# Kernel optimization log

Hardware: AMD Instinct MI355X
Metric: run time of the kernel (lower is better)

The kernel has to match this reference:

```python
import jax, jax.numpy as jnp
import numpy as np
import math

LN_EPS = 1e-5
EPS = 1e-8

def _unfold3(x, stride):
    # torch nn.Unfold(kernel_size=3, stride=stride, padding=1); output [B, C*9, L]
    B, C, H, W = x.shape
    xp = jnp.pad(x, ((0, 0), (0, 0), (1, 1), (1, 1)))
    Ho = (H + 2 - 3) // stride + 1
    Wo = (W + 2 - 3) // stride + 1
    pats = [xp[:, :, i:i + stride * (Ho - 1) + 1:stride, j:j + stride * (Wo - 1) + 1:stride]
            for i in range(3) for j in range(3)]
    out = jnp.stack(pats, axis=2)  # [B,C,9,Ho,Wo]  (c-major, then kh,kw: torch ordering)
    return out.reshape(B, C * 9, Ho * Wo)

def _ln(x, g, b):
    mu = jnp.mean(x, axis=-1, keepdims=True)
    var = jnp.mean((x - mu) ** 2, axis=-1, keepdims=True)
    return (x - mu) * jax.lax.rsqrt(var + LN_EPS) * g + b

def _prm_exp(x, w):
    # x: [B,T,emb], w: [m,emb] -> [B,T,m]
    m = w.shape[0]
    xd = jnp.sum(x * x, axis=-1, keepdims=True) / 2.0
    wtx = jnp.einsum('bte,me->btm', x, w)
    return jnp.exp(wtx - xd) / math.sqrt(m)

def _performer(x, kqv_w, kqv_b, pw, pb, g1, b1, g2, b2, m1w, m1b, m2w, m2b, w):
    # Token_performer.forward (dropout = identity, eval mode)
    h = _ln(x, g1, b1)
    kqv = h @ kqv_w.T + kqv_b
    k, q, v = jnp.split(kqv, 3, axis=-1)  # torch.split order: k, q, v
    kp = _prm_exp(k, w)
    qp = _prm_exp(q, w)
    D = jnp.einsum('btm,bm->bt', qp, kp.sum(axis=1))[..., None]        # [B,T,1]
    kptv = jnp.einsum('btn,btm->bnm', v, kp)                            # [B,emb,m]
    y = jnp.einsum('btm,bnm->btn', qp, kptv) / (D + EPS)                # [B,T,emb]
    y = v + (y @ pw.T + pb)
    h2 = _ln(y, g2, b2)
    mlp = jax.nn.gelu(h2 @ m1w.T + m1b, approximate=False) @ m2w.T + m2b
    return y + mlp

def _forward(x,
             p1_kqv_w, p1_kqv_b, p1_proj_w, p1_proj_b, p1_n1_g, p1_n1_b, p1_n2_g, p1_n2_b,
             p1_m1_w, p1_m1_b, p1_m2_w, p1_m2_b, p1_w,
             p2_kqv_w, p2_kqv_b, p2_proj_w, p2_proj_b, p2_n1_g, p2_n1_b, p2_n2_g, p2_n2_b,
             p2_m1_w, p2_m1_b, p2_m2_w, p2_m2_b, p2_w,
             proj_w, proj_b):
    t = _unfold3(x, 1).transpose(0, 2, 1)  # [B, 50176, 27]
    t = _performer(t, p1_kqv_w, p1_kqv_b, p1_proj_w, p1_proj_b, p1_n1_g, p1_n1_b,
                   p1_n2_g, p1_n2_b, p1_m1_w, p1_m1_b, p1_m2_w, p1_m2_b, p1_w)
    B, N, C = t.shape
    s = int(math.isqrt(N))
    t = t.transpose(0, 2, 1).reshape(B, C, s, s)
    t = _unfold3(t, 2).transpose(0, 2, 1)  # [B, 12544, 576]
    t = _performer(t, p2_kqv_w, p2_kqv_b, p2_proj_w, p2_proj_b, p2_n1_g, p2_n1_b,
                   p2_n2_g, p2_n2_b, p2_m1_w, p2_m1_b, p2_m2_w, p2_m2_b, p2_w)
    B, N, C = t.shape
    s = int(math.isqrt(N))
    t = t.transpose(0, 2, 1).reshape(B, C, s, s)
    t = _unfold3(t, 2).transpose(0, 2, 1)  # [B, 3136, 576]
    return t @ proj_w.T + proj_b           # [B, 3136, 768]

def setup_inputs() -> dict:
    key = jax.random.key(0)
    ks = iter(jax.random.split(key, 40))
    def rn(shape, scale=0.02):
        return (jax.random.normal(next(ks), shape, dtype=jnp.float32) * scale)
    EMB, M = 64, 32
    inp = {'x': jax.random.normal(next(ks), (8, 3, 224, 224), dtype=jnp.float32)}
    for pfx, dim in (('p1', 27), ('p2', 576)):
        inp[f'{pfx}_kqv_w'] = rn((3 * EMB, dim))
        inp[f'{pfx}_kqv_b'] = jnp.zeros((3 * EMB,), jnp.float32)
        inp[f'{pfx}_proj_w'] = rn((EMB, EMB))
        inp[f'{pfx}_proj_b'] = jnp.zeros((EMB,), jnp.float32)
        inp[f'{pfx}_n1_g'] = jnp.ones((dim,), jnp.float32)
        inp[f'{pfx}_n1_b'] = jnp.zeros((dim,), jnp.float32)
        inp[f'{pfx}_n2_g'] = jnp.ones((EMB,), jnp.float32)
        inp[f'{pfx}_n2_b'] = jnp.zeros((EMB,), jnp.float32)
        inp[f'{pfx}_m1_w'] = rn((EMB, EMB))
        inp[f'{pfx}_m1_b'] = jnp.zeros((EMB,), jnp.float32)
        inp[f'{pfx}_m2_w'] = rn((EMB, EMB))
        inp[f'{pfx}_m2_b'] = jnp.zeros((EMB,), jnp.float32)
        # frozen random-feature projection, scaled ~ orthogonal * sqrt(m)
        inp[f'{pfx}_w'] = jax.random.normal(next(ks), (M, EMB), dtype=jnp.float32)
    inp['proj_w'] = rn((768, 576))
    inp['proj_b'] = jnp.zeros((768,), jnp.float32)
    return inp

def reference(x,
              p1_kqv_w, p1_kqv_b, p1_proj_w, p1_proj_b, p1_n1_g, p1_n1_b, p1_n2_g, p1_n2_b,
              p1_m1_w, p1_m1_b, p1_m2_w, p1_m2_b, p1_w,
              p2_kqv_w, p2_kqv_b, p2_proj_w, p2_proj_b, p2_n1_g, p2_n1_b, p2_n2_g, p2_n2_b,
              p2_m1_w, p2_m1_b, p2_m2_w, p2_m2_b, p2_w,
              proj_w, proj_b):
    return _forward(x,
                    p1_kqv_w, p1_kqv_b, p1_proj_w, p1_proj_b, p1_n1_g, p1_n1_b, p1_n2_g, p1_n2_b,
                    p1_m1_w, p1_m1_b, p1_m2_w, p1_m2_b, p1_w,
                    p2_kqv_w, p2_kqv_b, p2_proj_w, p2_proj_b, p2_n1_g, p2_n1_b, p2_n2_g, p2_n2_b,
                    p2_m1_w, p2_m1_b, p2_m2_w, p2_m2_b, p2_w,
                    proj_w, proj_b)
```

## Files before the change

kernel.cpp:

```cpp
#include <hip/hip_runtime.h>
#include <hip/hip_bf16.h>
#include <math.h>

typedef __hip_bfloat16 bf16;
typedef __attribute__((ext_vector_type(8))) short frag8;
typedef __attribute__((ext_vector_type(4))) float f32x4;
typedef long long ll;

__device__ __forceinline__ float b2f(bf16 v) { return __bfloat162float(v); }
__device__ __forceinline__ bf16 f2b(float v) { return __float2bfloat16(v); }

__device__ __forceinline__ unsigned pk2f(float a, float b) {
    union { bf16 h[2]; unsigned u; } c;
    c.h[0] = f2b(a); c.h[1] = f2b(b);
    return c.u;
}
__device__ __forceinline__ void up8(const bf16* p, float* f) {
    const uint4 u = *(const uint4*)p;
    union { unsigned u; bf16 h[2]; } c;
    c.u = u.x; f[0] = b2f(c.h[0]); f[1] = b2f(c.h[1]);
    c.u = u.y; f[2] = b2f(c.h[0]); f[3] = b2f(c.h[1]);
    c.u = u.z; f[4] = b2f(c.h[0]); f[5] = b2f(c.h[1]);
    c.u = u.w; f[6] = b2f(c.h[0]); f[7] = b2f(c.h[1]);
}

#define LN_EPS 1e-5f
#define D_EPS 1e-8f
#define INV_SQRT_M 0.17677669529663687f

__global__ __launch_bounds__(256) void k_sniff(const void* x, int* mode)
{
    __shared__ int cnt;
    if (threadIdx.x == 0) cnt = 0;
    __syncthreads();
    const unsigned short* u = (const unsigned short*)x;
    const unsigned short h = u[2 * threadIdx.x];
    const unsigned int bits = ((unsigned int)h) << 16;
    const float v = __uint_as_float(bits);
    const float a = fabsf(v);
    const bool sane = (h == 0) || (a >= 1e-8f && a <= 1e4f);
    if (!sane) atomicAdd(&cnt, 1);
    __syncthreads();
    if (threadIdx.x == 0) *mode = (cnt > 64) ? 1 : 0;
}

struct CvTab { const void* src[28]; int dstOff[28]; int cum[29]; };

__global__ __launch_bounds__(256) void k_convert_all(CvTab tab, bf16* base,
                                                     const int* mode)
{
    const int idx = blockIdx.x * 256 + threadIdx.x;
    if (idx >= tab.cum[28]) return;
    int s = 0;
    while (idx >= tab.cum[s + 1]) ++s;
    const int local = idx - tab.cum[s];
    const float v = (*mode) ? ((const float*)tab.src[s])[local]
                            : b2f(((const bf16*)tab.src[s])[local]);
    base[tab.dstOff[s] + local] = f2b(v);
}

__global__ __launch_bounds__(256) void k_prep(
    const void* __restrict__ w1raw, const int* __restrict__ mode,
    bf16* __restrict__ w1ph, bf16* __restrict__ w1pl)
{
    const int idx = blockIdx.x * 256 + threadIdx.x;
    if (idx >= 6144) return;
    const int o = idx >> 5, k = idx & 31;
    float v = 0.f;
    if (k < 27)
        v = (*mode) ? ((const float*)w1raw)[o * 27 + k]
                    : b2f(((const bf16*)w1raw)[o * 27 + k]);
    const bf16 h = f2b(v);
    w1ph[idx] = h;
    w1pl[idx] = f2b(v - b2f(h));
}

__global__ __launch_bounds__(256) void k_fused1(
    const bf16* __restrict__ x, const bf16* __restrict__ w1ph,
    const bf16* __restrict__ w1pl, const bf16* __restrict__ kqvb,
    const bf16* __restrict__ n1g, const bf16* __restrict__ n1b,
    const bf16* __restrict__ pw,
    bf16* __restrict__ KP, bf16* __restrict__ QP, bf16* __restrict__ V,
    float* __restrict__ red, const int b)
{
    __shared__ __align__(16) char smem[49632];
    bf16 (*wps)[72] = (bf16(*)[72])(smem);
    bf16 (*Ah)[40]  = (bf16(*)[40])(smem + 4608);
    bf16 (*Al)[40]  = (bf16(*)[40])(smem + 9728);
    bf16 (*Th)[72]  = (bf16(*)[72])(smem + 14848);
    bf16 (*Tl)[72]  = (bf16(*)[72])(smem + 24064);
    bf16 (*Wh)[40]  = (bf16(*)[40])(smem + 33280);
    bf16 (*Wl)[40]  = (bf16(*)[40])(smem + 38400);
    bf16 (*KPs)[40] = (bf16(*)[40])(smem + 43520);
    bf16 (*Vs)[72]  = (bf16(*)[72])(smem + 14848);
    float* kbs = (float*)(smem + 48640);
    float* gs  = (float*)(smem + 49408);
    float* bs  = (float*)(smem + 49520);

    const int tid = threadIdx.x;
    {
        const int i = tid * 8;
        *(uint4*)(&wps[i >> 6][i & 63]) = *(const uint4*)(pw + i);
    }
    if (tid < 192) kbs[tid] = b2f(kqvb[tid]);
    if (tid < 27) { gs[tid] = b2f(n1g[tid]); bs[tid] = b2f(n1b[tid]); }
    if (blockIdx.x == 0)
        for (int i = tid; i < 2080; i += 256) red[i] = 0.f;

    const int tok = tid >> 2, part = tid & 3;
    const int t = blockIdx.x * 64 + tok;
    const int h = t / 224, w = t - h * 224;
    const int d0 = part * 7;
    const int nd = (part == 3) ? 6 : 7;
    float vals[7];
    float s = 0.f;
    #pragma unroll
    for (int q = 0; q < 7; ++q) {
        float val = 0.f;
        if (q < nd) {
            const int d = d0 + q;
            const int c = d / 9, rr = d - c * 9;
            const int pi = rr / 3, pj = rr - pi * 3;
            const int hh = h + pi - 1, ww = w + pj - 1;
            if (hh >= 0 && hh < 224 && ww >= 0 && ww < 224)
                val = b2f(x[((ll)(b * 3 + c) * 224 + hh) * 224 + ww]);
        }
        vals[q] = val; s += val;
    }
    s += __shfl_xor(s, 1, 64);  s += __shfl_xor(s, 2, 64);
    const float mean = s * (1.f / 27.f);
    float s2 = 0.f;
    #pragma unroll
    for (int q = 0; q < 7; ++q) {
        if (q < nd) { const float dd = vals[q] - mean; s2 += dd * dd; }
    }
    s2 += __shfl_xor(s2, 1, 64); s2 += __shfl_xor(s2, 2, 64);
    const float rs = rsqrtf(s2 * (1.f / 27.f) + LN_EPS);
    __syncthreads();
    #pragma unroll
    for (int q = 0; q < 7; ++q) {
        if (q < nd) {
            const int d = d0 + q;
            const float nv = (vals[q] - mean) * rs * gs[d] + bs[d];
            const bf16 nh = f2b(nv);
            Ah[tok][d] = nh;
            Al[tok][d] = f2b(nv - b2f(nh));
        }
    }
    if (part == 3) {
        #pragma unroll
        for (int d = 27; d < 32; ++d) { Ah[tok][d] = f2b(0.f); Al[tok][d] = f2b(0.f); }
    }

    const int wv = tid >> 6, lane = tid & 63;
    const int l15 = lane & 15;
    const int k8 = (lane >> 4) << 3;
    const int rbase = (lane >> 4) << 2;
    const int srow = tid >> 2;
    const int scol = (tid & 3) << 3;
    const int colg = (tid & 3) << 4;

    float xdK[4], xdQ[4];

    #pragma unroll
    for (int g = 0; g < 3; ++g) {
        *(uint4*)(&Wh[srow][scol]) = *(const uint4*)(w1ph + (g * 64 + srow) * 32 + scol);
        *(uint4*)(&Wl[srow][scol]) = *(const uint4*)(w1pl + (g * 64 + srow) * 32 + scol);
        __syncthreads();
        const frag8 ah = *(const frag8*)(&Ah[(wv << 4) + l15][k8]);
        const frag8 al = *(const frag8*)(&Al[(wv << 4) + l15][k8]);
        f32x4 acc[4] = {};
        #pragma unroll
        for (int nt = 0; nt < 4; ++nt) {
            const frag8 bh = *(const frag8*)(&Wh[(nt << 4) + l15][k8]);
            const frag8 bl = *(const frag8*)(&Wl[(nt << 4) + l15][k8]);
            acc[nt] = __builtin_amdgcn_mfma_f32_16x16x32_bf16(ah, bh, acc[nt], 0, 0, 0);
            acc[nt] = __builtin_amdgcn_mfma_f32_16x16x32_bf16(al, bh, acc[nt], 0, 0, 0);
            acc[nt] = __builtin_amdgcn_mfma_f32_16x16x32_bf16(ah, bl, acc[nt], 0, 0, 0);
            acc[nt] = __builtin_amdgcn_mfma_f32_16x16x32_bf16(al, bl, acc[nt], 0, 0, 0);
        }
        float xdp[4] = {0.f, 0.f, 0.f, 0.f};
        #pragma unroll
        for (int nt = 0; nt < 4; ++nt) {
            const int col = (nt << 4) + l15;
            const float bv = kbs[g * 64 + col];
            #pragma unroll
            for (int r = 0; r < 4; ++r) {
                const float tb = acc[nt][r] + bv;
                const int trow = (wv << 4) + rbase + r;
                if (g < 2) {
                    const bf16 th = f2b(tb);
                    Th[trow][col] = th;
                    Tl[trow][col] = f2b(tb - b2f(th));
                    xdp[r] += tb * tb;
                } else {
                    Vs[trow][col] = f2b(tb);
                }
            }
        }
        if (g < 2) {
            #pragma unroll
            for (int r = 0; r < 4; ++r) {
                float v = xdp[r];
                v += __shfl_xor(v, 1, 64); v += __shfl_xor(v, 2, 64);
                v += __shfl_xor(v, 4, 64); v += __shfl_xor(v, 8, 64);
                if (g == 0) xdK[r] = 0.5f * v; else xdQ[r] = 0.5f * v;
            }
        }
        __syncthreads();
        if (g < 2) {
            f32x4 acc2[2] = {};
            #pragma unroll
            for (int k0 = 0; k0 < 64; k0 += 32) {
                const frag8 ath = *(const frag8*)(&Th[(wv << 4) + l15][k8 + k0]);
                const frag8 atl = *(const frag8*)(&Tl[(wv << 4) + l15][k8 + k0]);
                #pragma unroll
                for (int nt = 0; nt < 2; ++nt) {
                    const frag8 bw = *(const frag8*)(&wps[(nt << 4) + l15][k8 + k0]);
                    acc2[nt] = __builtin_amdgcn_mfma_f32_16x16x32_bf16(ath, bw, acc2[nt], 0, 0, 0);
                    acc2[nt] = __builtin_amdgcn_mfma_f32_16x16x32_bf16(atl, bw, acc2[nt], 0, 0, 0);
                }
            }
            #pragma unroll
            for (int nt = 0; nt < 2; ++nt)
                #pragma unroll
                for (int r = 0; r < 4; ++r) {
                    const float xd = (g == 0) ? xdK[r] : xdQ[r];
                    const float p = expf(fminf(acc2[nt][r] - xd, 30.f)) * INV_SQRT_M;
                    KPs[(wv << 4) + rbase + r][(nt << 4) + l15] = f2b(p);
                }
            __syncthreads();
            bf16* dstP = (g == 0 ? KP : QP) + ((ll)blockIdx.x * 64 + srow) * 32 + scol;
            *(uint4*)dstP = *(const uint4*)(&KPs[srow][scol]);
            __syncthreads();
        } else {
            bf16* dstV = V + ((ll)blockIdx.x * 64 + srow) * 64 + colg;
            *(uint4*)dstV       = *(const uint4*)(&Vs[srow][colg]);
            *(uint4*)(dstV + 8) = *(const uint4*)(&Vs[srow][colg + 8]);
        }
    }
}

__global__ __launch_bounds__(256) void k_reduce(
    const bf16* __restrict__ kpB, const bf16* __restrict__ vB, const int vstride,
    const int T, float* __restrict__ redBase, const int chunk)
{
    __shared__ bf16 VT[64][72];
    __shared__ bf16 KT[32][72];
    const int bz = blockIdx.y;
    const bf16* kp = kpB + (ll)bz * T * 32;
    const bf16* v  = vB + (ll)bz * T * (ll)vstride;
    float* red = redBase + (ll)bz * 2080;
    const int tid = threadIdx.x;
    const int wv = tid >> 6, lane = tid & 63;
    const int l15 = lane & 15, k8 = (lane >> 4) << 3, rbase = (lane >> 4) << 2;
    const int t0 = blockIdx.x * chunk;

    frag8 ones;
    {
        union { bf16 h; short s; } u; u.h = f2b(1.f);
        #pragma unroll
        for (int i = 0; i < 8; ++i) ones[i] = u.s;
    }

    f32x4 acc[2] = {};
    f32x4 accK[2] = {};

    for (int tt = 0; tt < chunk; tt += 64) {
        const int tb = t0 + tt;
        __syncthreads();
        {
            const int tk = tid >> 2, n0 = (tid & 3) << 4;
            const bf16* src = v + (ll)(tb + tk) * vstride + n0;
            bf16 tmp[16];
            *(uint4*)tmp       = *(const uint4*)src;
            *(uint4*)(tmp + 8) = *(const uint4*)(src + 8);
            #pragma unroll
            for (int j = 0; j < 16; ++j) VT[n0 + j][tk] = tmp[j];
        }
        {
            const int tk = tid >> 2, m0 = (tid & 3) << 3;
            const bf16* src = kp + (ll)(tb + tk) * 32 + m0;
            bf16 tmp[8];
            *(uint4*)tmp = *(const uint4*)src;
            #pragma unroll
            for (int j = 0; j < 8; ++j) KT[m0 + j][tk] = tmp[j];
        }
        __syncthreads();
        #pragma unroll
        for (int ks = 0; ks < 2; ++ks) {
            const frag8 af = *(const frag8*)(&VT[(wv << 4) + l15][k8 + ks * 32]);
            #pragma unroll
            for (int tn = 0; tn < 2; ++tn) {
                const frag8 bfv = *(const frag8*)(&KT[(tn << 4) + l15][k8 + ks * 32]);
                acc[tn] = __builtin_amdgcn_mfma_f32_16x16x32_bf16(af, bfv, acc[tn], 0, 0, 0);
            }
            if (wv == 0) {
                #pragma unroll
                for (int tn = 0; tn < 2; ++tn) {
                    const frag8 bfv = *(const frag8*)(&KT[(tn << 4) + l15][k8 + ks * 32]);
                    accK[tn] = __builtin_amdgcn_mfma_f32_16x16x32_bf16(ones, bfv, accK[tn], 0, 0, 0);
                }
            }
        }
    }
    #pragma unroll
    for (int tn = 0; tn < 2; ++tn) {
        const int m = (tn << 4) + l15;
        #pragma unroll
        for (int r = 0; r < 4; ++r) {
            const int n = (wv << 4) + rbase + r;
            atomicAdd(&red[n * 32 + m], acc[tn][r]);
        }
    }
    if (wv == 0 && (lane >> 4) == 0) {
        #pragma unroll
        for (int tn = 0; tn < 2; ++tn)
            atomicAdd(&red[2048 + (tn << 4) + l15], accK[tn][0]);
    }
}

__global__ __launch_bounds__(256) void k_posta(
    const bf16* __restrict__ qpB, const float* __restrict__ redBase,
    const bf16* __restrict__ vB, const int vstride,
    const bf16* __restrict__ pw, const bf16* __restrict__ pb,
    bf16* outB, const int T)
{
    __shared__ __align__(16) char smem[46720];
    bf16 (*QPs)[40] = (bf16(*)[40])(smem);
    bf16 (*KH)[40]  = (bf16(*)[40])(smem + 5120);
    bf16 (*KL)[40]  = (bf16(*)[40])(smem + 10240);
    float (*Cs)[72] = (float(*)[72])(smem);
    bf16 (*PWs)[72] = (bf16(*)[72])(smem + 18432);
    bf16 (*Y0H)[72] = (bf16(*)[72])(smem + 27648);
    bf16 (*Y0L)[72] = (bf16(*)[72])(smem + 36864);
    float* invs  = (float*)(smem + 46080);
    float* pbs   = (float*)(smem + 46336);
    float* ksums = (float*)(smem + 46592);

    const int tid = threadIdx.x;
    const int bz = blockIdx.y;
    const float* red = redBase + (ll)bz * 2080;
    const bf16* qp = qpB + (ll)bz * (ll)T * 32;
    const bf16* v  = vB + (ll)bz * (ll)T * (ll)vstride;
    bf16* out = outB + (ll)bz * (ll)T * 64;
    const ll m0 = (ll)blockIdx.x * 64;

    {
        const int lr = tid >> 2, lc = (tid & 3) << 3;
        *(uint4*)(&QPs[lr][lc]) = *(const uint4*)(qp + (m0 + lr) * 32 + lc);
    }
    {
        const int lr = tid >> 2, lc = (tid & 3) << 4;
        *(uint4*)(&PWs[lr][lc])     = *(const uint4*)(pw + lr * 64 + lc);
        *(uint4*)(&PWs[lr][lc + 8]) = *(const uint4*)(pw + lr * 64 + lc + 8);
    }
    {
        const int i0 = tid * 8;
        const float4 a = *(const float4*)(red + i0);
        const float4 b = *(const float4*)(red + i0 + 4);
        const int n = i0 >> 5, m = i0 & 31;
        float xs[8] = {a.x, a.y, a.z, a.w, b.x, b.y, b.z, b.w};
        #pragma unroll
        for (int k = 0; k < 8; ++k) {
            const bf16 h = f2b(xs[k]);
            KH[n][m + k] = h;
            KL[n][m + k] = f2b(xs[k] - b2f(h));
        }
    }
    if (tid < 32) ksums[tid] = red[2048 + tid];
    if (tid < 64) pbs[tid] = b2f(pb[tid]);
    __syncthreads();

    if (tid < 64) {
        float D = D_EPS;
        #pragma unroll
        for (int m = 0; m < 32; ++m) D += b2f(QPs[tid][m]) * ksums[m];
        invs[tid] = 1.f / D;
    }

    const int wv = tid >> 6, lane = tid & 63;
    const int mr = (wv << 4) + (lane & 15);
    const int k8 = (lane >> 4) << 3;
    const int rbase = (lane >> 4) << 2;

    f32x4 acc[4] = {};
    {
        const frag8 af = *(const frag8*)(&QPs[mr][k8]);
        #pragma unroll
        for (int tn = 0; tn < 4; ++tn) {
            const int nr = (tn << 4) + (lane & 15);
            const frag8 bh = *(const frag8*)(&KH[nr][k8]);
            acc[tn] = __builtin_amdgcn_mfma_f32_16x16x32_bf16(af, bh, acc[tn], 0, 0, 0);
            const frag8 bl = *(const frag8*)(&KL[nr][k8]);
            acc[tn] = __builtin_amdgcn_mfma_f32_16x16x32_bf16(af, bl, acc[tn], 0, 0, 0);
        }
    }
    #pragma unroll
    for (int tn = 0; tn < 4; ++tn) {
        const int n = (tn << 4) + (lane & 15);
        #pragma unroll
        for (int r = 0; r < 4; ++r) {
            const float x = acc[tn][r];
            const bf16 h = f2b(x);
            Y0H[(wv << 4) + rbase + r][n] = h;
            Y0L[(wv << 4) + rbase + r][n] = f2b(x - b2f(h));
        }
    }
    __syncthreads();

    f32x4 acc2[4] = {};
    #pragma unroll
    for (int k0 = 0; k0 < 64; k0 += 32) {
        const frag8 ah = *(const frag8*)(&Y0H[mr][k8 + k0]);
        const frag8 al = *(const frag8*)(&Y0L[mr][k8 + k0]);
        #pragma unroll
        for (int tn = 0; tn < 4; ++tn) {
            const frag8 bw = *(const frag8*)(&PWs[(tn << 4) + (lane & 15)][k8 + k0]);
            acc2[tn] = __builtin_amdgcn_mfma_f32_16x16x32_bf16(ah, bw, acc2[tn], 0, 0, 0);
            acc2[tn] = __builtin_amdgcn_mfma_f32_16x16x32_bf16(al, bw, acc2[tn], 0, 0, 0);
        }
    }
    #pragma unroll
    for (int tn = 0; tn < 4; ++tn) {
        const int n = (tn << 4) + (lane & 15);
        #pragma unroll
        for (int r = 0; r < 4; ++r) {
            const int row = (wv << 4) + rbase + r;
            Cs[row][n] = acc2[tn][r] * invs[row] + pbs[n];
        }
    }
    __syncthreads();

    const int row = tid >> 2;
    const int colg = (tid & 3) << 4;
    const bf16* vsrc = v + (m0 + row) * (ll)vstride + colg;
    bf16* dst = out + (m0 + row) * 64 + colg;
    #pragma unroll
    for (int hh = 0; hh < 2; ++hh) {
        float vv[8];
        up8(vsrc + hh * 8, vv);
        const float* cp = &Cs[row][colg + hh * 8];
        uint4 st;
        st.x = pk2f(cp[0] + vv[0], cp[1] + vv[1]);
        st.y = pk2f(cp[2] + vv[2], cp[3] + vv[3]);
        st.z = pk2f(cp[4] + vv[4], cp[5] + vv[5]);
        st.w = pk2f(cp[6] + vv[6], cp[7] + vv[7]);
        *(uint4*)(dst + hh * 8) = st;
    }
}

__global__ __launch_bounds__(256) void k_mlpln(
    const bf16* H, const bf16* __restrict__ n2g, const bf16* __restrict__ n2b,
    const bf16* __restrict__ w1, const bf16* __restrict__ b1,
    const bf16* __restrict__ w2, const bf16* __restrict__ b2,
    const bf16* res, bf16* out)
{
    __shared__ bf16 Hs[64][72];
    __shared__ bf16 W1s[64][72];
    __shared__ bf16 W2s[64][72];
    __shared__ bf16 Gs[64][72];
    __shared__ float mns[64], rss[64];
    const int tid = threadIdx.x;
    const int wv = tid >> 6, lane = tid & 63;
    const ll m0 = (ll)blockIdx.x * 64;
    const int lr = tid >> 2;
    const int lc = (tid & 3) << 4;
    *(uint4*)(&Hs[lr][lc])      = *(const uint4*)(H + (m0 + lr) * 64 + lc);
    *(uint4*)(&Hs[lr][lc + 8])  = *(const uint4*)(H + (m0 + lr) * 64 + lc + 8);
    *(uint4*)(&W1s[lr][lc])     = *(const uint4*)(w1 + lr * 64 + lc);
    *(uint4*)(&W1s[lr][lc + 8]) = *(const uint4*)(w1 + lr * 64 + lc + 8);
    *(uint4*)(&W2s[lr][lc])     = *(const uint4*)(w2 + lr * 64 + lc);
    *(uint4*)(&W2s[lr][lc + 8]) = *(const uint4*)(w2 + lr * 64 + lc + 8);
    __syncthreads();
    if (tid < 64) {
        float s = 0.f, s2 = 0.f;
        #pragma unroll
        for (int n = 0; n < 64; ++n) { const float vv = b2f(Hs[tid][n]); s += vv; s2 += vv * vv; }
        const float mn = s * (1.f / 64.f);
        const float var = fmaxf(s2 * (1.f / 64.f) - mn * mn, 0.f);
        mns[tid] = mn; rss[tid] = rsqrtf(var + LN_EPS);
    }
    __syncthreads();
    for (int i = tid; i < 4096; i += 256) {
        const int r = i >> 6, c = i & 63;
        Hs[r][c] = f2b((b2f(Hs[r][c]) - mns[r]) * rss[r] * b2f(n2g[c]) + b2f(n2b[c]));
    }
    __syncthreads();
    const int mr = (wv << 4) + (lane & 15);
    const int k8 = (lane >> 4) << 3;
    const int rbase = (lane >> 4) << 2;
    f32x4 acc[4] = {};
    #pragma unroll
    for (int k0 = 0; k0 < 64; k0 += 32) {
        const frag8 af = *(const frag8*)(&Hs[mr][k8 + k0]);
        #pragma unroll
        for (int tn = 0; tn < 4; ++tn) {
            const frag8 bfv = *(const frag8*)(&W1s[(tn << 4) + (lane & 15)][k8 + k0]);
            acc[tn] = __builtin_amdgcn_mfma_f32_16x16x32_bf16(af, bfv, acc[tn], 0, 0, 0);
        }
    }
    #pragma unroll
    for (int tn = 0; tn < 4; ++tn) {
        const int n = (tn << 4) + (lane & 15);
        const float bv = b2f(b1[n]);
        #pragma unroll
        for (int r = 0; r < 4; ++r) {
            float v = acc[tn][r] + bv;
            v = 0.5f * v * (1.f + erff(v * 0.70710678118654752f));
            Gs[(wv << 4) + rbase + r][n] = f2b(v);
        }
    }
    __syncthreads();
    f32x4 acc2[4] = {};
    #pragma unroll
    for (int k0 = 0; k0 < 64; k0 += 32) {
        const frag8 af = *(const frag8*)(&Gs[mr][k8 + k0]);
        #pragma unroll
        for (int tn = 0; tn < 4; ++tn) {
            const frag8 bfv = *(const frag8*)(&W2s[(tn << 4) + (lane & 15)][k8 + k0]);
            acc2[tn] = __builtin_amdgcn_mfma_f32_16x16x32_bf16(af, bfv, acc2[tn], 0, 0, 0);
        }
    }
    #pragma unroll
    for (int tn = 0; tn < 4; ++tn) {
        const int n = (tn << 4) + (lane & 15);
        const float bv = b2f(b2[n]);
        #pragma unroll
        for (int r = 0; r < 4; ++r)
            Hs[(wv << 4) + rbase + r][n] = f2b(acc2[tn][r] + bv);
    }
    __syncthreads();
    const int row = tid >> 2;
    const int colg = (tid & 3) << 4;
    const bf16* rsrc = res + (m0 + row) * 64 + colg;
    bf16* dst = out + (m0 + row) * 64 + colg;
    #pragma unroll
    for (int hh = 0; hh < 2; ++hh) {
        float sv[8], rv[8];
        up8(&Hs[row][colg + hh * 8], sv);
        up8(rsrc + hh * 8, rv);
        uint4 st;
        st.x = pk2f(sv[0] + rv[0], sv[1] + rv[1]);
        st.y = pk2f(sv[2] + rv[2], sv[3] + rv[3]);
        st.z = pk2f(sv[4] + rv[4], sv[5] + rv[5]);
        st.w = pk2f(sv[6] + rv[6], sv[7] + rv[7]);
        *(uint4*)(dst + hh * 8) = st;
    }
}

__global__ __launch_bounds__(256) void k_unfold576(
    const bf16* __restrict__ in, const int Hin, const int Ho,
    const bf16* __restrict__ g, const bf16* __restrict__ bb,
    const int do_ln, bf16* __restrict__ A,
    const ll inBStride, const ll outBStride)
{
    in += (ll)blockIdx.y * inBStride;
    A  += (ll)blockIdx.y * outBStride;
    const int t = blockIdx.x * 4 + (threadIdx.x >> 6);
    const int l = threadIdx.x & 63;
    const int ho = t / Ho, wo = t - ho * Ho;
    float vals[9];
    float s = 0.f;
    #pragma unroll
    for (int r = 0; r < 9; ++r) {
        const int d = l + (r << 6);
        const int c = d / 9;
        const int rr = d - c * 9;
        const int i = rr / 3, j = rr - i * 3;
        const int hh = 2 * ho + i - 1, ww = 2 * wo + j - 1;
        float val = 0.f;
        if (hh >= 0 && hh < Hin && ww >= 0 && ww < Hin)
            val = b2f(in[((ll)hh * Hin + ww) * 64 + c]);
        vals[r] = val; s += val;
    }
    bf16* out = A + (ll)t * 576;
    if (do_ln) {
        #pragma unroll
        for (int o = 32; o > 0; o >>= 1) s += __shfl_xor(s, o, 64);
        const float mean = s * (1.f / 576.f);
        float s2 = 0.f;
        #pragma unroll
        for (int r = 0; r < 9; ++r) { const float dd = vals[r] - mean; s2 += dd * dd; }
        #pragma unroll
        for (int o = 32; o > 0; o >>= 1) s2 += __shfl_xor(s2, o, 64);
        const float rs = rsqrtf(s2 * (1.f / 576.f) + LN_EPS);
        #pragma unroll
        for (int r = 0; r < 9; ++r) {
            const int d = l + (r << 6);
            out[d] = f2b((vals[r] - mean) * rs * b2f(g[d]) + b2f(bb[d]));
        }
    } else {
        #pragma unroll
        for (int r = 0; r < 9; ++r) out[l + (r << 6)] = f2b(vals[r]);
    }
}

__global__ __launch_bounds__(256) void k_gemm(
    const bf16* __restrict__ A, const int lda,
    const bf16* __restrict__ W,
    const bf16* __restrict__ bias,
    const bf16* res, const int ldres,
    void* C, const int ldc, const ll mOff,
    const int K, const int* outm)
{
    __shared__ bf16 As[2][64][40];
    __shared__ bf16 Bs[2][64][40];
    __shared__ bf16 Cs[64][72];
    const int tid = threadIdx.x;
    const int wv = tid >> 6;
    const int lane = tid & 63;
    const ll m0 = (ll)blockIdx.x * 64;
    const int n0 = blockIdx.y * 64;
    f32x4 acc[4] = {};
    const int lr = tid >> 2;
    const int lc = (tid & 3) << 3;
    const int mr = (wv << 4) + (lane & 15);
    const int k8 = (lane >> 4) << 3;
    const bf16* Ag = A + (m0 + lr) * (ll)lda + lc;
    const bf16* Wg = W + (ll)(n0 + lr) * K + lc;

    uint4 av  = *(const uint4*)(Ag);
    uint4 wv4 = *(const uint4*)(Wg);
    *(uint4*)(&As[0][lr][lc]) = av;
    *(uint4*)(&Bs[0][lr][lc]) = wv4;
    int cur = 0;
    __syncthreads();
    for (int k0 = 0; k0 < K; k0 += 32) {
        const bool nxt = (k0 + 32 < K);
        if (nxt) {
            av  = *(const uint4*)(Ag + k0 + 32);
            wv4 = *(const uint4*)(Wg + k0 + 32);
        }
        const frag8 af = *(const frag8*)(&As[cur][mr][k8]);
        #pragma unroll
        for (int tn = 0; tn < 4; ++tn) {
            const frag8 bfv = *(const frag8*)(&Bs[cur][(tn << 4) + (lane & 15)][k8]);
            acc[tn] = __builtin_amdgcn_mfma_f32_16x16x32_bf16(af, bfv, acc[tn], 0, 0, 0);
        }
        if (nxt) {
            *(uint4*)(&As[cur ^ 1][lr][lc]) = av;
            *(uint4*)(&Bs[cur ^ 1][lr][lc]) = wv4;
        }
        __syncthreads();
        cur ^= 1;
    }
    const int om = outm ? *outm : 0;
    const int rbase = (lane >> 4) << 2;
    if (om) {
        #pragma unroll
        for (int tn = 0; tn < 4; ++tn) {
            const int n = n0 + (tn << 4) + (lane & 15);
            const float bv = bias ? b2f(bias[n]) : 0.f;
            #pragma unroll
            for (int r = 0; r < 4; ++r) {
                const ll m = m0 + (wv << 4) + rbase + r;
                float v = acc[tn][r] + bv;
                if (res) v += b2f(res[m * (ll)ldres + n]);
                ((float*)C)[(m + mOff) * (ll)ldc + n] = v;
            }
        }
        return;
    }
    #pragma unroll
    for (int tn = 0; tn < 4; ++tn) {
        const int nl = (tn << 4) + (lane & 15);
        const float bv = bias ? b2f(bias[n0 + nl]) : 0.f;
        #pragma unroll
        for (int r = 0; r < 4; ++r) {
            const ll m = m0 + (wv << 4) + rbase + r;
            float v = acc[tn][r] + bv;
            if (res) v += b2f(res[m * (ll)ldres + n0 + nl]);
            Cs[(wv << 4) + rbase + r][nl] = f2b(v);
        }
    }
    __syncthreads();
    const int row = tid >> 2;
    const int colg = (tid & 3) << 4;
    bf16* dst = (bf16*)C + (m0 + mOff + row) * (ll)ldc + n0 + colg;
    *(uint4*)dst       = *(const uint4*)(&Cs[row][colg]);
    *(uint4*)(dst + 8) = *(const uint4*)(&Cs[row][colg + 8]);
}

__global__ __launch_bounds__(256) void k_fusedP2(
    const bf16* __restrict__ kqv, const bf16* __restrict__ pw,
    bf16* __restrict__ KP, bf16* __restrict__ QP,
    float* __restrict__ redBase, const int T)
{
    __shared__ float wps[2048];
    const int tid = threadIdx.x;
    const int bz = blockIdx.y;
    for (int i = tid; i < 2048; i += 256) wps[i] = b2f(pw[i]);
    if (blockIdx.x == 0) {
        float* red = redBase + (ll)bz * 2080;
        for (int i = tid; i < 2080; i += 256) red[i] = 0.f;
    }
    __syncthreads();
    const ll gt = (ll)bz * T + blockIdx.x * 256 + tid;
    const bf16* row = kqv + gt * 192;
    float xv[64];
    float p32[32];
    #pragma unroll
    for (int g = 0; g < 8; ++g) up8(row + g * 8, xv + g * 8);
    float xd = 0.f;
    #pragma unroll
    for (int e = 0; e < 64; ++e) xd += xv[e] * xv[e];
    xd *= 0.5f;
    #pragma unroll 4
    for (int m = 0; m < 32; ++m) {
        float a = -xd;
        #pragma unroll
        for (int e = 0; e < 64; ++e) a += xv[e] * wps[m * 64 + e];
        p32[m] = expf(fminf(a, 30.f)) * INV_SQRT_M;
    }
    #pragma unroll
    for (int g = 0; g < 4; ++g) {
        uint4 st;
        st.x = pk2f(p32[g * 8 + 0], p32[g * 8 + 1]);
        st.y = pk2f(p32[g * 8 + 2], p32[g * 8 + 3]);
        st.z = pk2f(p32[g * 8 + 4], p32[g * 8 + 5]);
        st.w = pk2f(p32[g * 8 + 6], p32[g * 8 + 7]);
        *(uint4*)(KP + gt * 32 + g * 8) = st;
    }
    #pragma unroll
    for (int g = 0; g < 8; ++g) up8(row + 64 + g * 8, xv + g * 8);
    xd = 0.f;
    #pragma unroll
    for (int e = 0; e < 64; ++e) xd += xv[e] * xv[e];
    xd *= 0.5f;
    #pragma unroll 4
    for (int m = 0; m < 32; ++m) {
        float a = -xd;
        #pragma unroll
        for (int e = 0; e < 64; ++e) a += xv[e] * wps[m * 64 + e];
        p32[m] = expf(fminf(a, 30.f)) * INV_SQRT_M;
    }
    #pragma unroll
    for (int g = 0; g < 4; ++g) {
        uint4 st;
        st.x = pk2f(p32[g * 8 + 0], p32[g * 8 + 1]);
        st.y = pk2f(p32[g * 8 + 2], p32[g * 8 + 3]);
        st.z = pk2f(p32[g * 8 + 4], p32[g * 8 + 5]);
        st.w = pk2f(p32[g * 8 + 6], p32[g * 8 + 7]);
        *(uint4*)(QP + gt * 32 + g * 8) = st;
    }
}

extern "C" void kernel_launch(void* const* d_in, const int* in_sizes, int n_in,
                              void* d_out, int out_size, void* d_ws, size_t ws_size,
                              hipStream_t stream)
{
    (void)in_sizes; (void)n_in; (void)out_size; (void)ws_size;
    const int T1 = 50176, T2 = 12544;
    char* ws = (char*)d_ws;

    size_t cur = 0;
    auto alloc = [&](size_t bytes) {
        size_t r = cur; cur += (bytes + 127) & ~(size_t)127; return r;
    };
    static const int segIdx[28] = {0, 2, 3, 4, 5, 6, 7, 8, 9, 10, 11, 12, 13,
                                   14, 15, 16, 17, 18, 19, 20, 21, 22, 23, 24, 25, 26, 27, 28};
    static const int segN[28] = {1204224, 192, 4096, 64, 27, 27, 64, 64, 4096, 64, 4096, 64, 2048,
                                 110592, 192, 4096, 64, 576, 576, 64, 64, 4096, 64, 4096, 64, 2048,
                                 442368, 768};
    size_t segOff[28];
    for (int i = 0; i < 28; ++i) segOff[i] = alloc((size_t)segN[i] * 2);
    const size_t oMODE = alloc(256);
    const size_t oRED  = alloc(66560);
    const size_t oW1P  = alloc(24576);
    const size_t oBIG  = alloc(6422528);
    const size_t oKP   = alloc(3211264);
    const size_t oQP   = alloc(3211264);
    (void)oQP;

    bf16* P[28];
    for (int i = 0; i < 28; ++i) P[i] = (bf16*)(ws + segOff[i]);
    bf16* XC = P[0];
    bf16 *P1KQVB = P[1], *P1PW = P[2], *P1PB = P[3], *P1N1G = P[4], *P1N1B = P[5];
    bf16 *P1N2G = P[6], *P1N2B = P[7], *P1M1W = P[8], *P1M1B = P[9], *P1M2W = P[10];
    bf16 *P1M2B = P[11], *P1W = P[12];
    bf16 *P2KQVW = P[13], *P2KQVB = P[14], *P2PW = P[15], *P2PB = P[16];
    bf16 *P2N1G = P[17], *P2N1B = P[18], *P2N2G = P[19], *P2N2B = P[20];
    bf16 *P2M1W = P[21], *P2M1B = P[22], *P2M2W = P[23], *P2M2B = P[24], *P2W = P[25];
    bf16 *PROJW = P[26], *PROJB = P[27];

    int*   MODE = (int*)(ws + oMODE);
    float* REDF = (float*)(ws + oRED);
    bf16*  W1PH = (bf16*)(ws + oW1P);
    bf16*  W1PL = (bf16*)(ws + oW1P + 12288);
    bf16*  BIG  = (bf16*)(ws + oBIG);
    bf16*  KP   = (bf16*)(ws + oKP);
    bf16*  QP   = (bf16*)(ws + oKP + 3211264);
    bf16*  A2   = (bf16*)(ws + oKP);
    bf16*  KQV2F = (bf16*)d_out;
    bf16*  KP2F  = (bf16*)(ws + oKP);
    bf16*  QP2F  = (bf16*)(ws + oKP + 6422528);
    bf16*  YB2F  = (bf16*)(ws + oBIG);
    bf16*  A3c   = (bf16*)(ws + oBIG + 12845056);

    k_sniff<<<1, 256, 0, stream>>>(d_in[0], MODE);
    CvTab tab;
    int cum = 0;
    for (int i = 0; i < 28; ++i) {
        tab.src[i] = d_in[segIdx[i]];
        tab.dstOff[i] = (int)(segOff[i] / 2);
        tab.cum[i] = cum;
        cum += segN[i];
    }
    tab.cum[28] = cum;
    k_convert_all<<<(cum + 255) / 256, 256, 0, stream>>>(tab, (bf16*)ws, MODE);
    k_prep<<<24, 256, 0, stream>>>(d_in[1], MODE, W1PH, W1PL);

    for (int b = 0; b < 8; ++b) {
        float* REDb = REDF + (ll)b * 2080;
        k_fused1<<<784, 256, 0, stream>>>(XC, W1PH, W1PL, P1KQVB, P1N1G, P1N1B,
                                          P1W, KP, QP, BIG, REDb, b);
        k_reduce<<<dim3(392, 1), 256, 0, stream>>>(KP, BIG, 64, T1, REDb, 128);
        k_posta<<<dim3(784, 1), 256, 0, stream>>>(QP, REDb, BIG, 64, P1PW, P1PB,
                                                  BIG, T1);
        k_mlpln<<<784, 256, 0, stream>>>(BIG, P1N2G, P1N2B, P1M1W, P1M1B,
                                         P1M2W, P1M2B, BIG, BIG);
        k_unfold576<<<dim3(3136, 1), 256, 0, stream>>>(BIG, 224, 112, P2N1G, P2N1B,
                                                       1, A2, 0, 0);
        k_gemm<<<dim3(196, 3), 256, 0, stream>>>(A2, 576, P2KQVW, P2KQVB,
            nullptr, 0, KQV2F, 192, (ll)b * T2, 576, nullptr);
    }

    k_fusedP2<<<dim3(49, 8), 256, 0, stream>>>(KQV2F, P2W, KP2F, QP2F, REDF, T2);
    k_reduce<<<dim3(98, 8), 256, 0, stream>>>(KP2F, KQV2F + 128, 192, T2, REDF, 128);
    k_posta<<<dim3(196, 8), 256, 0, stream>>>(QP2F, REDF, KQV2F + 128, 192,
                                              P2PW, P2PB, YB2F, T2);
    k_mlpln<<<1568, 256, 0, stream>>>(YB2F, P2N2G, P2N2B, P2M1W, P2M1B,
                                      P2M2W, P2M2B, YB2F, YB2F);

    for (int c = 0; c < 4; ++c) {
        k_unfold576<<<dim3(784, 2), 256, 0, stream>>>(
            YB2F + (ll)(2 * c) * T2 * 64, 112, 56, nullptr, nullptr, 0,
            A3c, (ll)T2 * 64, (ll)3136 * 576);
        k_gemm<<<dim3(98, 12), 256, 0, stream>>>(A3c, 576, PROJW, PROJB,
            nullptr, 0, d_out, 768, (ll)c * 6272, 576, MODE);
    }
}
```

Baseline: 1.045 ms.

## Fuse attention post-process with MLP+LN, MFMA-ize stage-2 features, batch final projection

Merges k_posta and k_mlpln into one kernel that keeps the residual output in shared memory, removing a global round trip and a launch per stage. k_fusedP2 replaces its per-thread scalar 64x32 dot products with bf16 MFMA over 64-row tiles, run on a 4x larger grid. When the workspace is big enough, the final unfold+projection runs as one full-size launch instead of four chunks. The cost is more shared-memory aliasing, and the feature projection weights are now rounded to bf16 inside MFMA instead of being used in fp32.

```diff
diff --git a/kernel.cpp b/kernel.cpp
--- a/kernel.cpp
+++ b/kernel.cpp
@@ -17,6 +17,13 @@
 }
 __device__ __forceinline__ void up8(const bf16* p, float* f) {
     const uint4 u = *(const uint4*)p;
+    union { unsigned u; bf16 h[2]; } c;
+    c.u = u.x; f[0] = b2f(c.h[0]); f[1] = b2f(c.h[1]);
+    c.u = u.y; f[2] = b2f(c.h[0]); f[3] = b2f(c.h[1]);
+    c.u = u.z; f[4] = b2f(c.h[0]); f[5] = b2f(c.h[1]);
+    c.u = u.w; f[6] = b2f(c.h[0]); f[7] = b2f(c.h[1]);
+}
+__device__ __forceinline__ void up8u(const uint4 u, float* f) {
     union { unsigned u; bf16 h[2]; } c;
     c.u = u.x; f[0] = b2f(c.h[0]); f[1] = b2f(c.h[1]);
     c.u = u.y; f[2] = b2f(c.h[0]); f[3] = b2f(c.h[1]);
@@ -320,23 +327,33 @@
     }
 }
 
-__global__ __launch_bounds__(256) void k_posta(
+__global__ __launch_bounds__(256) void k_postmlp(
     const bf16* __restrict__ qpB, const float* __restrict__ redBase,
     const bf16* __restrict__ vB, const int vstride,
     const bf16* __restrict__ pw, const bf16* __restrict__ pb,
+    const bf16* __restrict__ n2g, const bf16* __restrict__ n2b,
+    const bf16* __restrict__ w1, const bf16* __restrict__ b1,
+    const bf16* __restrict__ w2, const bf16* __restrict__ b2,
     bf16* outB, const int T)
 {
-    __shared__ __align__(16) char smem[46720];
+    __shared__ __align__(16) char smem[47232];
     bf16 (*QPs)[40] = (bf16(*)[40])(smem);
     bf16 (*KH)[40]  = (bf16(*)[40])(smem + 5120);
     bf16 (*KL)[40]  = (bf16(*)[40])(smem + 10240);
     float (*Cs)[72] = (float(*)[72])(smem);
+    bf16 (*W1s)[72] = (bf16(*)[72])(smem);
+    bf16 (*W2s)[72] = (bf16(*)[72])(smem + 9216);
     bf16 (*PWs)[72] = (bf16(*)[72])(smem + 18432);
+    bf16 (*Gs)[72]  = (bf16(*)[72])(smem + 18432);
     bf16 (*Y0H)[72] = (bf16(*)[72])(smem + 27648);
+    bf16 (*Ys)[72]  = (bf16(*)[72])(smem + 27648);
     bf16 (*Y0L)[72] = (bf16(*)[72])(smem + 36864);
+    bf16 (*Hn)[72]  = (bf16(*)[72])(smem + 36864);
     float* invs  = (float*)(smem + 46080);
     float* pbs   = (float*)(smem + 46336);
     float* ksums = (float*)(smem + 46592);
+    float* mns   = (float*)(smem + 46720);
+    float* rss   = (float*)(smem + 46976);
 
     const int tid = threadIdx.x;
     const int bz = blockIdx.y;
@@ -346,15 +363,13 @@
     bf16* out = outB + (ll)bz * (ll)T * 64;
     const ll m0 = (ll)blockIdx.x * 64;
 
-    {
-        const int lr = tid >> 2, lc = (tid & 3) << 3;
-        *(uint4*)(&QPs[lr][lc]) = *(const uint4*)(qp + (m0 + lr) * 32 + lc);
-    }
-    {
-        const int lr = tid >> 2, lc = (tid & 3) << 4;
-        *(uint4*)(&PWs[lr][lc])     = *(const uint4*)(pw + lr * 64 + lc);
-        *(uint4*)(&PWs[lr][lc + 8]) = *(const uint4*)(pw + lr * 64 + lc + 8);
-    }
+    const int lr = tid >> 2;
+    const int lc8 = (tid & 3) << 3;
+    const int lc16 = (tid & 3) << 4;
+
+    *(uint4*)(&QPs[lr][lc8]) = *(const uint4*)(qp + (m0 + lr) * 32 + lc8);
+    *(uint4*)(&PWs[lr][lc16])     = *(const uint4*)(pw + lr * 64 + lc16);
+    *(uint4*)(&PWs[lr][lc16 + 8]) = *(const uint4*)(pw + lr * 64 + lc16 + 8);
     {
         const int i0 = tid * 8;
         const float4 a = *(const float4*)(red + i0);
@@ -380,7 +395,8 @@
     }
 
     const int wv = tid >> 6, lane = tid & 63;
-    const int mr = (wv << 4) + (lane & 15);
+    const int l15 = lane & 15;
+    const int mr = (wv << 4) + l15;
     const int k8 = (lane >> 4) << 3;
     const int rbase = (lane >> 4) << 2;
 
@@ -389,7 +405,7 @@
         const frag8 af = *(const frag8*)(&QPs[mr][k8]);
         #pragma unroll
         for (int tn = 0; tn < 4; ++tn) {
-            const int nr = (tn << 4) + (lane & 15);
+            const int nr = (tn << 4) + l15;
             const frag8 bh = *(const frag8*)(&KH[nr][k8]);
             acc[tn] = __builtin_amdgcn_mfma_f32_16x16x32_bf16(af, bh, acc[tn], 0, 0, 0);
             const frag8 bl = *(const frag8*)(&KL[nr][k8]);
@@ -398,7 +414,7 @@
     }
     #pragma unroll
     for (int tn = 0; tn < 4; ++tn) {
-        const int n = (tn << 4) + (lane & 15);
+        const int n = (tn << 4) + l15;
         #pragma unroll
         for (int r = 0; r < 4; ++r) {
             const float x = acc[tn][r];
@@ -416,14 +432,14 @@
         const frag8 al = *(const frag8*)(&Y0L[mr][k8 + k0]);
         #pragma unroll
         for (int tn = 0; tn < 4; ++tn) {
-            const frag8 bw = *(const frag8*)(&PWs[(tn << 4) + (lane & 15)][k8 + k0]);
+            const frag8 bw = *(const frag8*)(&PWs[(tn << 4) + l15][k8 + k0]);
             acc2[tn] = __builtin_amdgcn_mfma_f32_16x16x32_bf16(ah, bw, acc2[tn], 0, 0, 0);
             acc2[tn] = __builtin_amdgcn_mfma_f32_16x16x32_bf16(al, bw, acc2[tn], 0, 0, 0);
         }
     }
     #pragma unroll
     for (int tn = 0; tn < 4; ++tn) {
-        const int n = (tn << 4) + (lane & 15);
+        const int n = (tn << 4) + l15;
         #pragma unroll
         for (int r = 0; r < 4; ++r) {
             const int row = (wv << 4) + rbase + r;
@@ -432,120 +448,102 @@
     }
     __syncthreads();
 
-    const int row = tid >> 2;
-    const int colg = (tid & 3) << 4;
-    const bf16* vsrc = v + (m0 + row) * (ll)vstride + colg;
-    bf16* dst = out + (m0 + row) * 64 + colg;
-    #pragma unroll
-    for (int hh = 0; hh < 2; ++hh) {
-        float vv[8];
-        up8(vsrc + hh * 8, vv);
-        const float* cp = &Cs[row][colg + hh * 8];
-        uint4 st;
-        st.x = pk2f(cp[0] + vv[0], cp[1] + vv[1]);
-        st.y = pk2f(cp[2] + vv[2], cp[3] + vv[3]);
-        st.z = pk2f(cp[4] + vv[4], cp[5] + vv[5]);
-        st.w = pk2f(cp[6] + vv[6], cp[7] + vv[7]);
-        *(uint4*)(dst + hh * 8) = st;
-    }
-}
-
-__global__ __launch_bounds__(256) void k_mlpln(
-    const bf16* H, const bf16* __restrict__ n2g, const bf16* __restrict__ n2b,
-    const bf16* __restrict__ w1, const bf16* __restrict__ b1,
-    const bf16* __restrict__ w2, const bf16* __restrict__ b2,
-    const bf16* res, bf16* out)
-{
-    __shared__ bf16 Hs[64][72];
-    __shared__ bf16 W1s[64][72];
-    __shared__ bf16 W2s[64][72];
-    __shared__ bf16 Gs[64][72];
-    __shared__ float mns[64], rss[64];
-    const int tid = threadIdx.x;
-    const int wv = tid >> 6, lane = tid & 63;
-    const ll m0 = (ll)blockIdx.x * 64;
-    const int lr = tid >> 2;
-    const int lc = (tid & 3) << 4;
-    *(uint4*)(&Hs[lr][lc])      = *(const uint4*)(H + (m0 + lr) * 64 + lc);
-    *(uint4*)(&Hs[lr][lc + 8])  = *(const uint4*)(H + (m0 + lr) * 64 + lc + 8);
-    *(uint4*)(&W1s[lr][lc])     = *(const uint4*)(w1 + lr * 64 + lc);
-    *(uint4*)(&W1s[lr][lc + 8]) = *(const uint4*)(w1 + lr * 64 + lc + 8);
-    *(uint4*)(&W2s[lr][lc])     = *(const uint4*)(w2 + lr * 64 + lc);
-    *(uint4*)(&W2s[lr][lc + 8]) = *(const uint4*)(w2 + lr * 64 + lc + 8);
-    __syncthreads();
+    {
+        const int row = tid >> 2;
+        const bf16* vsrc = v + (m0 + row) * (ll)vstride + lc16;
+        #pragma unroll
+        for (int hh = 0; hh < 2; ++hh) {
+            float vv[8];
+            up8(vsrc + hh * 8, vv);
+            const float* cp = &Cs[row][lc16 + hh * 8];
+            uint4 st;
+            st.x = pk2f(cp[0] + vv[0], cp[1] + vv[1]);
+            st.y = pk2f(cp[2] + vv[2], cp[3] + vv[3]);
+            st.z = pk2f(cp[4] + vv[4], cp[5] + vv[5]);
+            st.w = pk2f(cp[6] + vv[6], cp[7] + vv[7]);
+            *(uint4*)(&Ys[row][lc16 + hh * 8]) = st;
+        }
+    }
+    __syncthreads();
+
     if (tid < 64) {
         float s = 0.f, s2 = 0.f;
         #pragma unroll
-        for (int n = 0; n < 64; ++n) { const float vv = b2f(Hs[tid][n]); s += vv; s2 += vv * vv; }
+        for (int n = 0; n < 64; ++n) { const float vv = b2f(Ys[tid][n]); s += vv; s2 += vv * vv; }
         const float mn = s * (1.f / 64.f);
         const float var = fmaxf(s2 * (1.f / 64.f) - mn * mn, 0.f);
         mns[tid] = mn; rss[tid] = rsqrtf(var + LN_EPS);
     }
-    __syncthreads();
+    *(uint4*)(&W1s[lr][lc16])     = *(const uint4*)(w1 + lr * 64 + lc16);
+    *(uint4*)(&W1s[lr][lc16 + 8]) = *(const uint4*)(w1 + lr * 64 + lc16 + 8);
+    *(uint4*)(&W2s[lr][lc16])     = *(const uint4*)(w2 + lr * 64 + lc16);
+    *(uint4*)(&W2s[lr][lc16 + 8]) = *(const uint4*)(w2 + lr * 64 + lc16 + 8);
+    __syncthreads();
+
     for (int i = tid; i < 4096; i += 256) {
         const int r = i >> 6, c = i & 63;
-        Hs[r][c] = f2b((b2f(Hs[r][c]) - mns[r]) * rss[r] * b2f(n2g[c]) + b2f(n2b[c]));
-    }
-    __syncthreads();
-    const int mr = (wv << 4) + (lane & 15);
-    const int k8 = (lane >> 4) << 3;
-    const int rbase = (lane >> 4) << 2;
-    f32x4 acc[4] = {};
+        Hn[r][c] = f2b((b2f(Ys[r][c]) - mns[r]) * rss[r] * b2f(n2g[c]) + b2f(n2b[c]));
+    }
+    __syncthreads();
+
+    f32x4 accm[4] = {};
     #pragma unroll
     for (int k0 = 0; k0 < 64; k0 += 32) {
-        const frag8 af = *(const frag8*)(&Hs[mr][k8 + k0]);
+        const frag8 af = *(const frag8*)(&Hn[mr][k8 + k0]);
         #pragma unroll
         for (int tn = 0; tn < 4; ++tn) {
-            const frag8 bfv = *(const frag8*)(&W1s[(tn << 4) + (lane & 15)][k8 + k0]);
-            acc[tn] = __builtin_amdgcn_mfma_f32_16x16x32_bf16(af, bfv, acc[tn], 0, 0, 0);
+            const frag8 bfv = *(const frag8*)(&W1s[(tn << 4) + l15][k8 + k0]);
+            accm[tn] = __builtin_amdgcn_mfma_f32_16x16x32_bf16(af, bfv, accm[tn], 0, 0, 0);
         }
     }
     #pragma unroll
     for (int tn = 0; tn < 4; ++tn) {
-        const int n = (tn << 4) + (lane & 15);
+        const int n = (tn << 4) + l15;
         const float bv = b2f(b1[n]);
         #pragma unroll
         for (int r = 0; r < 4; ++r) {
-            float v = acc[tn][r] + bv;
-            v = 0.5f * v * (1.f + erff(v * 0.70710678118654752f));
-            Gs[(wv << 4) + rbase + r][n] = f2b(v);
-        }
-    }
-    __syncthreads();
-    f32x4 acc2[4] = {};
+            float vg = accm[tn][r] + bv;
+            vg = 0.5f * vg * (1.f + erff(vg * 0.70710678118654752f));
+            Gs[(wv << 4) + rbase + r][n] = f2b(vg);
+        }
+    }
+    __syncthreads();
+
+    f32x4 accn[4] = {};
     #pragma unroll
     for (int k0 = 0; k0 < 64; k0 += 32) {
         const frag8 af = *(const frag8*)(&Gs[mr][k8 + k0]);
         #pragma unroll
         for (int tn = 0; tn < 4; ++tn) {
-            const frag8 bfv = *(const frag8*)(&W2s[(tn << 4) + (lane & 15)][k8 + k0]);
-            acc2[tn] = __builtin_amdgcn_mfma_f32_16x16x32_bf16(af, bfv, acc2[tn], 0, 0, 0);
+            const frag8 bfv = *(const frag8*)(&W2s[(tn << 4) + l15][k8 + k0]);
+            accn[tn] = __builtin_amdgcn_mfma_f32_16x16x32_bf16(af, bfv, accn[tn], 0, 0, 0);
         }
     }
     #pragma unroll
     for (int tn = 0; tn < 4; ++tn) {
-        const int n = (tn << 4) + (lane & 15);
+        const int n = (tn << 4) + l15;
         const float bv = b2f(b2[n]);
         #pragma unroll
         for (int r = 0; r < 4; ++r)
-            Hs[(wv << 4) + rbase + r][n] = f2b(acc2[tn][r] + bv);
-    }
-    __syncthreads();
-    const int row = tid >> 2;
-    const int colg = (tid & 3) << 4;
-    const bf16* rsrc = res + (m0 + row) * 64 + colg;
-    bf16* dst = out + (m0 + row) * 64 + colg;
-    #pragma unroll
-    for (int hh = 0; hh < 2; ++hh) {
-        float sv[8], rv[8];
-        up8(&Hs[row][colg + hh * 8], sv);
-        up8(rsrc + hh * 8, rv);
-        uint4 st;
-        st.x = pk2f(sv[0] + rv[0], sv[1] + rv[1]);
-        st.y = pk2f(sv[2] + rv[2], sv[3] + rv[3]);
-        st.z = pk2f(sv[4] + rv[4], sv[5] + rv[5]);
-        st.w = pk2f(sv[6] + rv[6], sv[7] + rv[7]);
-        *(uint4*)(dst + hh * 8) = st;
+            Hn[(wv << 4) + rbase + r][n] = f2b(accn[tn][r] + bv);
+    }
+    __syncthreads();
+
+    {
+        const int row = tid >> 2;
+        bf16* dst = out + (m0 + row) * 64 + lc16;
+        #pragma unroll
+        for (int hh = 0; hh < 2; ++hh) {
+            float sv[8], rv[8];
+            up8(&Hn[row][lc16 + hh * 8], sv);
+            up8(&Ys[row][lc16 + hh * 8], rv);
+            uint4 st;
+            st.x = pk2f(sv[0] + rv[0], sv[1] + rv[1]);
+            st.y = pk2f(sv[2] + rv[2], sv[3] + rv[3]);
+            st.z = pk2f(sv[4] + rv[4], sv[5] + rv[5]);
+            st.w = pk2f(sv[6] + rv[6], sv[7] + rv[7]);
+            *(uint4*)(dst + hh * 8) = st;
+        }
     }
 }
 
@@ -687,62 +685,66 @@
     bf16* __restrict__ KP, bf16* __restrict__ QP,
     float* __restrict__ redBase, const int T)
 {
-    __shared__ float wps[2048];
+    __shared__ __align__(16) char smem[19200];
+    bf16 (*Ks)[72]  = (bf16(*)[72])(smem);
+    bf16 (*wps)[72] = (bf16(*)[72])(smem + 9216);
+    bf16 (*KPs)[40] = (bf16(*)[40])(smem + 13824);
+    float* xds = (float*)(smem + 18944);
+
     const int tid = threadIdx.x;
     const int bz = blockIdx.y;
-    for (int i = tid; i < 2048; i += 256) wps[i] = b2f(pw[i]);
+    {
+        const int i = tid * 8;
+        *(uint4*)(&wps[i >> 6][i & 63]) = *(const uint4*)(pw + i);
+    }
     if (blockIdx.x == 0) {
         float* red = redBase + (ll)bz * 2080;
         for (int i = tid; i < 2080; i += 256) red[i] = 0.f;
     }
-    __syncthreads();
-    const ll gt = (ll)bz * T + blockIdx.x * 256 + tid;
-    const bf16* row = kqv + gt * 192;
-    float xv[64];
-    float p32[32];
-    #pragma unroll
-    for (int g = 0; g < 8; ++g) up8(row + g * 8, xv + g * 8);
-    float xd = 0.f;
-    #pragma unroll
-    for (int e = 0; e < 64; ++e) xd += xv[e] * xv[e];
-    xd *= 0.5f;
-    #pragma unroll 4
-    for (int m = 0; m < 32; ++m) {
-        float a = -xd;
-        #pragma unroll
-        for (int e = 0; e < 64; ++e) a += xv[e] * wps[m * 64 + e];
-        p32[m] = expf(fminf(a, 30.f)) * INV_SQRT_M;
-    }
-    #pragma unroll
-    for (int g = 0; g < 4; ++g) {
-        uint4 st;
-        st.x = pk2f(p32[g * 8 + 0], p32[g * 8 + 1]);
-        st.y = pk2f(p32[g * 8 + 2], p32[g * 8 + 3]);
-        st.z = pk2f(p32[g * 8 + 4], p32[g * 8 + 5]);
-        st.w = pk2f(p32[g * 8 + 6], p32[g * 8 + 7]);
-        *(uint4*)(KP + gt * 32 + g * 8) = st;
-    }
-    #pragma unroll
-    for (int g = 0; g < 8; ++g) up8(row + 64 + g * 8, xv + g * 8);
-    xd = 0.f;
-    #pragma unroll
-    for (int e = 0; e < 64; ++e) xd += xv[e] * xv[e];
-    xd *= 0.5f;
-    #pragma unroll 4
-    for (int m = 0; m < 32; ++m) {
-        float a = -xd;
-        #pragma unroll
-        for (int e = 0; e < 64; ++e) a += xv[e] * wps[m * 64 + e];
-        p32[m] = expf(fminf(a, 30.f)) * INV_SQRT_M;
-    }
-    #pragma unroll
-    for (int g = 0; g < 4; ++g) {
-        uint4 st;
-        st.x = pk2f(p32[g * 8 + 0], p32[g * 8 + 1]);
-        st.y = pk2f(p32[g * 8 + 2], p32[g * 8 + 3]);
-        st.z = pk2f(p32[g * 8 + 4], p32[g * 8 + 5]);
-        st.w = pk2f(p32[g * 8 + 6], p32[g * 8 + 7]);
-        *(uint4*)(QP + gt * 32 + g * 8) = st;
+    const ll gt0 = (ll)bz * T + (ll)blockIdx.x * 64;
+    const int srow = tid >> 2;
+    const int colg = (tid & 3) << 4;
+    const int scol = (tid & 3) << 3;
+    const int wv = tid >> 6, lane = tid & 63;
+    const int l15 = lane & 15, k8 = (lane >> 4) << 3, rbase = (lane >> 4) << 2;
+
+    #pragma unroll
+    for (int p = 0; p < 2; ++p) {
+        const bf16* src = kqv + (gt0 + srow) * 192 + p * 64 + colg;
+        const uint4 u0 = *(const uint4*)src;
+        const uint4 u1 = *(const uint4*)(src + 8);
+        *(uint4*)(&Ks[srow][colg])     = u0;
+        *(uint4*)(&Ks[srow][colg + 8]) = u1;
+        float f0[8], f1[8];
+        up8u(u0, f0); up8u(u1, f1);
+        float s2 = 0.f;
+        #pragma unroll
+        for (int k = 0; k < 8; ++k) s2 += f0[k] * f0[k] + f1[k] * f1[k];
+        s2 += __shfl_xor(s2, 1, 64); s2 += __shfl_xor(s2, 2, 64);
+        if ((tid & 3) == 0) xds[srow] = 0.5f * s2;
+        __syncthreads();
+        f32x4 acc2[2] = {};
+        #pragma unroll
+        for (int k0 = 0; k0 < 64; k0 += 32) {
+            const frag8 af = *(const frag8*)(&Ks[(wv << 4) + l15][k8 + k0]);
+            #pragma unroll
+            for (int nt = 0; nt < 2; ++nt) {
+                const frag8 bw = *(const frag8*)(&wps[(nt << 4) + l15][k8 + k0]);
+                acc2[nt] = __builtin_amdgcn_mfma_f32_16x16x32_bf16(af, bw, acc2[nt], 0, 0, 0);
+            }
+        }
+        #pragma unroll
+        for (int nt = 0; nt < 2; ++nt)
+            #pragma unroll
+            for (int r = 0; r < 4; ++r) {
+                const int trow = (wv << 4) + rbase + r;
+                const float pv = expf(fminf(acc2[nt][r] - xds[trow], 30.f)) * INV_SQRT_M;
+                KPs[trow][(nt << 4) + l15] = f2b(pv);
+            }
+        __syncthreads();
+        bf16* dst = (p == 0 ? KP : QP) + (gt0 + srow) * 32 + scol;
+        *(uint4*)dst = *(const uint4*)(&KPs[srow][scol]);
+        __syncthreads();
     }
 }
 
@@ -750,7 +752,7 @@
                               void* d_out, int out_size, void* d_ws, size_t ws_size,
                               hipStream_t stream)
 {
-    (void)in_sizes; (void)n_in; (void)out_size; (void)ws_size;
+    (void)in_sizes; (void)n_in; (void)out_size;
     const int T1 = 50176, T2 = 12544;
     char* ws = (char*)d_ws;
 
@@ -816,28 +818,33 @@
         k_fused1<<<784, 256, 0, stream>>>(XC, W1PH, W1PL, P1KQVB, P1N1G, P1N1B,
                                           P1W, KP, QP, BIG, REDb, b);
         k_reduce<<<dim3(392, 1), 256, 0, stream>>>(KP, BIG, 64, T1, REDb, 128);
-        k_posta<<<dim3(784, 1), 256, 0, stream>>>(QP, REDb, BIG, 64, P1PW, P1PB,
-                                                  BIG, T1);
-        k_mlpln<<<784, 256, 0, stream>>>(BIG, P1N2G, P1N2B, P1M1W, P1M1B,
-                                         P1M2W, P1M2B, BIG, BIG);
+        k_postmlp<<<dim3(784, 1), 256, 0, stream>>>(QP, REDb, BIG, 64, P1PW, P1PB,
+            P1N2G, P1N2B, P1M1W, P1M1B, P1M2W, P1M2B, BIG, T1);
         k_unfold576<<<dim3(3136, 1), 256, 0, stream>>>(BIG, 224, 112, P2N1G, P2N1B,
                                                        1, A2, 0, 0);
         k_gemm<<<dim3(196, 3), 256, 0, stream>>>(A2, 576, P2KQVW, P2KQVB,
             nullptr, 0, KQV2F, 192, (ll)b * T2, 576, nullptr);
     }
 
-    k_fusedP2<<<dim3(49, 8), 256, 0, stream>>>(KQV2F, P2W, KP2F, QP2F, REDF, T2);
+    k_fusedP2<<<dim3(196, 8), 256, 0, stream>>>(KQV2F, P2W, KP2F, QP2F, REDF, T2);
     k_reduce<<<dim3(98, 8), 256, 0, stream>>>(KP2F, KQV2F + 128, 192, T2, REDF, 128);
-    k_posta<<<dim3(196, 8), 256, 0, stream>>>(QP2F, REDF, KQV2F + 128, 192,
-                                              P2PW, P2PB, YB2F, T2);
-    k_mlpln<<<1568, 256, 0, stream>>>(YB2F, P2N2G, P2N2B, P2M1W, P2M1B,
-                                      P2M2W, P2M2B, YB2F, YB2F);
-
-    for (int c = 0; c < 4; ++c) {
-        k_unfold576<<<dim3(784, 2), 256, 0, stream>>>(
-            YB2F + (ll)(2 * c) * T2 * 64, 112, 56, nullptr, nullptr, 0,
-            A3c, (ll)T2 * 64, (ll)3136 * 576);
-        k_gemm<<<dim3(98, 12), 256, 0, stream>>>(A3c, 576, PROJW, PROJB,
-            nullptr, 0, d_out, 768, (ll)c * 6272, 576, MODE);
-    }
-}
+    k_postmlp<<<dim3(196, 8), 256, 0, stream>>>(QP2F, REDF, KQV2F + 128, 192,
+        P2PW, P2PB, P2N2G, P2N2B, P2M1W, P2M1B, P2M2W, P2M2B, YB2F, T2);
+
+    const size_t needFull = oBIG + 12845056 + (size_t)25088 * 576 * 2;
+    if (ws_size >= needFull) {
+        bf16* A3 = (bf16*)(ws + oBIG + 12845056);
+        k_unfold576<<<dim3(784, 8), 256, 0, stream>>>(
+            YB2F, 112, 56, nullptr, nullptr, 0, A3, (ll)T2 * 64, (ll)3136 * 576);
+        k_gemm<<<dim3(392, 12), 256, 0, stream>>>(A3, 576, PROJW, PROJB,
+            nullptr, 0, d_out, 768, 0, 576, MODE);
+    } else {
+        for (int c = 0; c < 4; ++c) {
+            k_unfold576<<<dim3(784, 2), 256, 0, stream>>>(
+                YB2F + (ll)(2 * c) * T2 * 64, 112, 56, nullptr, nullptr, 0,
+                A3c, (ll)T2 * 64, (ll)3136 * 576);
+            k_gemm<<<dim3(98, 12), 256, 0, stream>>>(A3c, 576, PROJW, PROJB,
+                nullptr, 0, d_out, 768, (ll)c * 6272, 576, MODE);
+        }
+    }
+}
```

New measurement: 974.0 us. 1.07x faster.
